# Performance work log

Measured on AMD Instinct MI355X. Metric: run time of the kernel, lower is better.

Reference implementation:

```python
import jax, jax.numpy as jnp
import numpy as np
import math

B, T, C, H = 4, 2048, 1024, 16
D = C // H  # head dim = 64

def setup_inputs() -> dict:
    key = jax.random.key(0)
    k1, k2, k3 = jax.random.split(key, 3)
    scale = 0.02
    return {
        "x": jax.random.normal(k1, (B, T, C), dtype=jnp.float32),
        "W_qkv": jax.random.normal(k2, (C, 3 * C), dtype=jnp.float32) * scale,
        "b_qkv": jnp.zeros((3 * C,), dtype=jnp.float32),
        "W_proj": jax.random.normal(k3, (C, C), dtype=jnp.float32) * scale,
        "b_proj": jnp.zeros((C,), dtype=jnp.float32),
    }

def reference(x, W_qkv, b_qkv, W_proj, b_proj):
    Bx, Tx, Cx = x.shape
    qkv = x @ W_qkv + b_qkv                      # [B, T, 3C]
    q, k, v = jnp.split(qkv, 3, axis=-1)
    # [B, T, C] -> [B, H, T, D]
    q = q.reshape(Bx, Tx, H, D).transpose(0, 2, 1, 3)
    k = k.reshape(Bx, Tx, H, D).transpose(0, 2, 1, 3)
    v = v.reshape(Bx, Tx, H, D).transpose(0, 2, 1, 3)
    scores = jnp.einsum("bhqd,bhkd->bhqk", q, k) * (1.0 / math.sqrt(D))
    causal = jnp.tril(jnp.ones((Tx, Tx), dtype=bool))  # [T, T]
    scores = jnp.where(causal[None, None, :, :], scores, jnp.finfo(scores.dtype).min)
    attn = jax.nn.softmax(scores, axis=-1)
    # dropout(p=0.1) in the original is stochastic; omitted for a deterministic baseline
    out = jnp.einsum("bhqk,bhkd->bhqd", attn, v)   # [B, H, T, D]
    out = out.transpose(0, 2, 1, 3).reshape(Bx, Tx, Cx)
    return out @ W_proj + b_proj
```

## Files before the change

### kernel.cpp

```cpp
#include <hip/hip_runtime.h>
#include <hip/hip_bf16.h>
#include <cstdint>
#include <cstddef>

#define Bsz 4
#define Tseq 2048
#define Cdim 1024
#define Hh 16
#define Dh 64

typedef unsigned short u16;
typedef __bf16 bfx8 __attribute__((ext_vector_type(8)));
typedef float f32x4 __attribute__((ext_vector_type(4)));
typedef float f32x16 __attribute__((ext_vector_type(16)));
typedef unsigned short u16x8 __attribute__((ext_vector_type(8)));

#define AS1 __attribute__((address_space(1)))
#define AS3 __attribute__((address_space(3)))

#define QSCALE 0.18033688f

__device__ __forceinline__ u16 f2b(float f) {
  union { float f; unsigned u; } x; x.f = f;
  unsigned r = x.u + 0x7FFFu + ((x.u >> 16) & 1u);
  return (u16)(r >> 16);
}
__device__ __forceinline__ float b2f(u16 b) {
  union { unsigned u; float f; } x; x.u = ((unsigned)b) << 16; return x.f;
}
__device__ __forceinline__ unsigned cvtpk(float lo, float hi) {
  unsigned r;
  asm("v_cvt_pk_bf16_f32 %0, %1, %2" : "=v"(r) : "v"(lo), "v"(hi));
  return r;
}
__device__ __forceinline__ void swap32(unsigned &a, unsigned &b) {
  asm("v_permlane32_swap_b32 %0, %1" : "+v"(a), "+v"(b));
}

__global__ __launch_bounds__(256) void cvt_f32_bf16(const float* __restrict__ in,
                                                    u16* __restrict__ out, int n4) {
  int i = blockIdx.x * 256 + threadIdx.x;
  if (i < n4) {
    const float4 v = reinterpret_cast<const float4*>(in)[i];
    ushort4 o;
    o.x = f2b(v.x); o.y = f2b(v.y); o.z = f2b(v.z); o.w = f2b(v.w);
    reinterpret_cast<ushort4*>(out)[i] = o;
  }
}

__global__ __launch_bounds__(256) void transpose_cvt(const float* __restrict__ in,
                                                     u16* __restrict__ out, int R, int Cn) {
  __shared__ float tile[32][33];
  const int c0 = blockIdx.x * 32, r0 = blockIdx.y * 32;
  const int tx = threadIdx.x, ty = threadIdx.y;
  for (int i = ty; i < 32; i += 8)
    tile[i][tx] = in[(size_t)(r0 + i) * Cn + c0 + tx];
  __syncthreads();
  for (int i = ty; i < 32; i += 8)
    out[(size_t)(c0 + i) * R + r0 + tx] = f2b(tile[tx][i]);
}

template<int MODE>
__global__ __launch_bounds__(512, 4) void gemm_bt(const u16* __restrict__ A, const u16* __restrict__ Bt,
                                                  const float* __restrict__ bias, void* __restrict__ Cout,
                                                  u16* __restrict__ vtout,
                                                  int M, int N, int K) {
  __shared__ __align__(16) u16 Alds[3][4096];
  __shared__ __align__(16) u16 Blds[3][8192];
  const int tid = threadIdx.x;
  const int lane = tid & 63;
  const int wid = tid >> 6;
  const int nwgx = gridDim.x;
  const int nwg = nwgx * gridDim.y;
  int lin = blockIdx.y * nwgx + blockIdx.x;
  lin = (lin & 7) * (nwg >> 3) + (lin >> 3);
  const int mbase = (lin / nwgx) * 128;
  const int nbase = (lin % nwgx) * 256;
  const int wm = wid & 1, wn = wid >> 1;

  const int sLlow = lane >> 3;
  const int s8 = (lane & 7) ^ sLlow;
  const int srow = 2 * (wid * 8 + sLlow) + (s8 >> 2);
  const int skof = (s8 & 3) * 8;

  const u16* pa  = A  + (size_t)(mbase + srow) * K + skof;
  const u16* pb0 = Bt + (size_t)(nbase + srow) * K + skof;
  const u16* pb1 = pb0 + (size_t)128 * K;

  const int raA = wm * 64 + (lane & 15);
  const int LA = raA >> 1;
  const int pA = ((raA & 1) * 4 + (lane >> 4)) ^ (LA & 7);
  const int aoffw = LA * 64 + pA * 8;
  const int rbB = wn * 64 + (lane & 15);
  const int LB = rbB >> 1;
  const int pB = ((rbB & 1) * 4 + (lane >> 4)) ^ (LB & 7);
  const int boffw = LB * 64 + pB * 8;

  AS3 u16* aldsb = (AS3 u16*)&Alds[0][0];
  AS3 u16* bldsb = (AS3 u16*)&Blds[0][0];

  const f32x4 vzero = {0.f, 0.f, 0.f, 0.f};
  f32x4 acc[4][4];
  #pragma unroll
  for (int i = 0; i < 4; ++i)
    #pragma unroll
    for (int j = 0; j < 4; ++j) acc[i][j] = vzero;

  const int NT = K >> 5;

  auto stage = [&](int slot) {
    __builtin_amdgcn_global_load_lds((AS1 void*)const_cast<u16*>(pa),
                                     (AS3 void*)&Alds[slot][wid * 512], 16, 0, 0);
    __builtin_amdgcn_global_load_lds((AS1 void*)const_cast<u16*>(pb0),
                                     (AS3 void*)&Blds[slot][wid * 512], 16, 0, 0);
    __builtin_amdgcn_global_load_lds((AS1 void*)const_cast<u16*>(pb1),
                                     (AS3 void*)&Blds[slot][4096 + wid * 512], 16, 0, 0);
    pa += 32; pb0 += 32; pb1 += 32;
  };

  stage(0);
  stage(1);
  asm volatile("s_waitcnt vmcnt(3)" ::: "memory");
  __builtin_amdgcn_s_barrier();

  int slot = 0, pf = 2;
  for (int t = 0; t < NT; ++t) {
    if (t + 2 < NT) stage(pf);

    bfx8 af[4], bfv[4];
    {
      AS3 u16* ap = aldsb + slot * 4096 + aoffw;
      AS3 u16* bp = bldsb + slot * 8192 + boffw;
      asm volatile("ds_read_b128 %0, %1"             : "=v"(af[0])  : "v"(ap));
      asm volatile("ds_read_b128 %0, %1 offset:1024" : "=v"(af[1])  : "v"(ap));
      asm volatile("ds_read_b128 %0, %1"             : "=v"(bfv[0]) : "v"(bp));
      asm volatile("ds_read_b128 %0, %1 offset:1024" : "=v"(bfv[1]) : "v"(bp));
      asm volatile("ds_read_b128 %0, %1 offset:2048" : "=v"(bfv[2]) : "v"(bp));
      asm volatile("ds_read_b128 %0, %1 offset:3072" : "=v"(bfv[3]) : "v"(bp));
      asm volatile("ds_read_b128 %0, %1 offset:2048" : "=v"(af[2])  : "v"(ap));
      asm volatile("ds_read_b128 %0, %1 offset:3072" : "=v"(af[3])  : "v"(ap));
    }
    asm volatile("s_waitcnt lgkmcnt(2)" ::: "memory");
    __builtin_amdgcn_sched_barrier(0);

    __builtin_amdgcn_s_setprio(1);
    #pragma unroll
    for (int mf = 0; mf < 2; ++mf)
      #pragma unroll
      for (int nf = 0; nf < 4; ++nf)
        acc[mf][nf] = __builtin_amdgcn_mfma_f32_16x16x32_bf16(af[mf], bfv[nf], acc[mf][nf], 0, 0, 0);
    __builtin_amdgcn_s_setprio(0);

    asm volatile("s_waitcnt lgkmcnt(0)" ::: "memory");
    __builtin_amdgcn_sched_barrier(0);

    __builtin_amdgcn_s_setprio(1);
    #pragma unroll
    for (int mf = 2; mf < 4; ++mf)
      #pragma unroll
      for (int nf = 0; nf < 4; ++nf)
        acc[mf][nf] = __builtin_amdgcn_mfma_f32_16x16x32_bf16(af[mf], bfv[nf], acc[mf][nf], 0, 0, 0);
    __builtin_amdgcn_s_setprio(0);

    if (t + 2 < NT)      { asm volatile("s_waitcnt vmcnt(3)" ::: "memory"); }
    else if (t + 1 < NT) { asm volatile("s_waitcnt vmcnt(0)" ::: "memory"); }
    if (t + 1 < NT) __builtin_amdgcn_s_barrier();

    slot = (slot == 2) ? 0 : slot + 1;
    pf   = (pf == 2) ? 0 : pf + 1;
  }

  float bv[4];
  #pragma unroll
  for (int nf = 0; nf < 4; ++nf) bv[nf] = bias[nbase + wn * 64 + nf * 16 + (lane & 15)];
  #pragma unroll
  for (int mf = 0; mf < 4; ++mf) {
    #pragma unroll
    for (int nf = 0; nf < 4; ++nf) {
      const int r0 = mbase + wm * 64 + mf * 16 + (lane >> 4) * 4;
      const int c  = nbase + wn * 64 + nf * 16 + (lane & 15);
      const int cb = nbase + wn * 64 + nf * 16;
      const float cscale = (MODE == 1 && cb >= 1024 && cb < 2048) ? QSCALE : 1.0f;
      float v[4];
      #pragma unroll
      for (int j = 0; j < 4; ++j) v[j] = (acc[mf][nf][j] + bv[nf]) * cscale;
      if (MODE == 1 && cb >= 2048) {
        const int hh = (c - 2048) >> 6, dd = (c - 2048) & 63;
        const int bb = r0 >> 11, tt = r0 & 2047;
        ushort4 pkd;
        pkd.x = f2b(v[0]); pkd.y = f2b(v[1]); pkd.z = f2b(v[2]); pkd.w = f2b(v[3]);
        *reinterpret_cast<ushort4*>(
            &vtout[(((size_t)bb * Hh + hh) * Dh + dd) * Tseq + tt]) = pkd;
      } else {
        #pragma unroll
        for (int j = 0; j < 4; ++j) {
          if (MODE == 1) ((u16*)Cout)[(size_t)(r0 + j) * N + c] = f2b(v[j]);
          else           ((float*)Cout)[(size_t)(r0 + j) * N + c] = v[j];
        }
      }
    }
  }
}

#define ROWI(r) (((r) & 3) + 8 * ((r) >> 2))
__global__ __launch_bounds__(512, 4) void attn_fwd(const u16* __restrict__ qkv,
                                                   const u16* __restrict__ vt,
                                                   u16* __restrict__ aout) {
  __shared__ __align__(16) u16 Klds[4][64 * 64];
  __shared__ __align__(16) u16 Vtlds[4][64 * 64];
  const int tid = threadIdx.x;
  const int lane = tid & 63;
  const int wid = tid >> 6;
  const int qg = wid & 3;
  const int half = wid >> 2;
  const int lin = blockIdx.y * gridDim.x + blockIdx.x;
  const int bh = (lin & 7) * 8 + ((lin >> 3) & 7);
  const int qpair = lin >> 6;
  const int b = bh >> 4, h = bh & 15;
  const int hi4 = (lane & 32) >> 3;

  const int stg_row = lane >> 3;
  const int stg_srcslot = (lane & 7) ^ (stg_row & 7);

  const u16* gkbase = qkv + ((size_t)b * Tseq + wid * 8 + stg_row) * 3072
                      + 1024 + h * 64 + stg_srcslot * 8;
  const u16* gvbase = vt + ((size_t)bh * Dh + wid * 8 + stg_row) * Tseq + stg_srcslot * 8;

  float* Olds = reinterpret_cast<float*>(&Klds[0][0]);
  float* Llds = reinterpret_cast<float*>(&Vtlds[0][0]);

  #pragma unroll 1
  for (int pass = 0; pass < 2; ++pass) {
    const int qtile = pass ? qpair : (15 - qpair);
    const int qwb = qtile * 128 + qg * 32;
    const int ntiles = qtile * 2 + 2;

    bfx8 qf[4];
    {
      const int qrow = qwb + (lane & 31);
      #pragma unroll
      for (int c = 0; c < 4; ++c) {
        const u16* src = qkv + (size_t)(b * Tseq + qrow) * 3072 + h * 64 + c * 16 + (hi4 << 1);
        qf[c] = *reinterpret_cast<const bfx8*>(src);
      }
    }

    float l_r = 0.f;
    f32x16 o0, o1;
    #pragma unroll
    for (int r = 0; r < 16; ++r) { o0[r] = 0.f; o1[r] = 0.f; }

    auto stageT = [&](int t) {
      const u16* gk = gkbase + (size_t)t * 64 * 3072;
      const u16* gv = gvbase + t * 64;
      __builtin_amdgcn_global_load_lds((AS1 void*)const_cast<u16*>(gk),
                                       (AS3 void*)&Klds[t & 3][wid * 512], 16, 0, 0);
      __builtin_amdgcn_global_load_lds((AS1 void*)const_cast<u16*>(gv),
                                       (AS3 void*)&Vtlds[t & 3][wid * 512], 16, 0, 0);
    };
    stageT(0);
    stageT(1);
    __syncthreads();

    for (int t = 0; t < ntiles; t += 2) {
      if (t + 2 < ntiles) stageT(t + 2);
      if (t + 3 < ntiles) stageT(t + 3);

      const int tt = t + half;
      const int kb = tt * 64;
      const int buf = tt & 3;
      if (kb <= qwb + 31) {
        f32x16 st0, st1;
        #pragma unroll
        for (int r = 0; r < 16; ++r) { st0[r] = 0.f; st1[r] = 0.f; }
        __builtin_amdgcn_s_setprio(1);
        #pragma unroll
        for (int c = 0; c < 4; ++c) {
          const int row0 = lane & 31;
          const int sl = (c * 2 + (lane >> 5)) ^ (row0 & 7);
          const bfx8 k0 = *reinterpret_cast<const bfx8*>(&Klds[buf][row0 * 64 + sl * 8]);
          const bfx8 k1 = *reinterpret_cast<const bfx8*>(&Klds[buf][(row0 + 32) * 64 + sl * 8]);
          st0 = __builtin_amdgcn_mfma_f32_32x32x16_bf16(k0, qf[c], st0, 0, 0, 0);
          st1 = __builtin_amdgcn_mfma_f32_32x32x16_bf16(k1, qf[c], st1, 0, 0, 0);
        }
        __builtin_amdgcn_s_setprio(0);

        if (kb + 63 > qwb) {
          const int qg_ = qwb + (lane & 31);
          #pragma unroll
          for (int r = 0; r < 16; ++r) {
            const int kt = kb + ROWI(r) + hi4;
            if (kt > qg_) st0[r] = -1e30f;
            if (kt + 32 > qg_) st1[r] = -1e30f;
          }
        }

        float rs = 0.f;
        #pragma unroll
        for (int r = 0; r < 16; ++r) { st0[r] = exp2f(st0[r]); rs += st0[r]; }
        #pragma unroll
        for (int r = 0; r < 16; ++r) { st1[r] = exp2f(st1[r]); rs += st1[r]; }
        rs += __shfl_xor(rs, 32);
        l_r += rs;

        bfx8 pf[4];
        #pragma unroll
        for (int tph = 0; tph < 2; ++tph) {
          #pragma unroll
          for (int c2 = 0; c2 < 2; ++c2) {
            const int rb = c2 * 8;
            float s0 = tph ? st1[rb + 0] : st0[rb + 0], s1 = tph ? st1[rb + 1] : st0[rb + 1];
            float s2 = tph ? st1[rb + 2] : st0[rb + 2], s3 = tph ? st1[rb + 3] : st0[rb + 3];
            float s4 = tph ? st1[rb + 4] : st0[rb + 4], s5 = tph ? st1[rb + 5] : st0[rb + 5];
            float s6 = tph ? st1[rb + 6] : st0[rb + 6], s7 = tph ? st1[rb + 7] : st0[rb + 7];
            unsigned w0 = cvtpk(s0, s1);
            unsigned w2 = cvtpk(s4, s5);
            swap32(w0, w2);
            unsigned w1 = cvtpk(s2, s3);
            unsigned w3 = cvtpk(s6, s7);
            swap32(w1, w3);
            union { unsigned w[4]; bfx8 v; } u;
            u.w[0] = w0; u.w[1] = w1; u.w[2] = w2; u.w[3] = w3;
            pf[tph * 2 + c2] = u.v;
          }
        }

        __builtin_amdgcn_s_setprio(1);
        #pragma unroll
        for (int c4 = 0; c4 < 4; ++c4) {
          const int vrow = lane & 31;
          const int sl = (c4 * 2 + (lane >> 5)) ^ (vrow & 7);
          const bfx8 vf0 = *reinterpret_cast<const bfx8*>(&Vtlds[buf][vrow * 64 + sl * 8]);
          const bfx8 vf1 = *reinterpret_cast<const bfx8*>(&Vtlds[buf][(vrow + 32) * 64 + sl * 8]);
          o0 = __builtin_amdgcn_mfma_f32_32x32x16_bf16(pf[c4], vf0, o0, 0, 0, 0);
          o1 = __builtin_amdgcn_mfma_f32_32x32x16_bf16(pf[c4], vf1, o1, 0, 0, 0);
        }
        __builtin_amdgcn_s_setprio(0);
      }

      __syncthreads();
    }

    if (half == 1) {
      Llds[qg * 64 + lane] = l_r;
      #pragma unroll
      for (int r = 0; r < 16; ++r) {
        Olds[qg * 2048 + r * 64 + lane]        = o0[r];
        Olds[qg * 2048 + (r + 16) * 64 + lane] = o1[r];
      }
    }
    __syncthreads();
    if (half == 0) {
      const float l1 = Llds[qg * 64 + lane];
      const float linv = 1.0f / (l_r + l1);
      #pragma unroll
      for (int r = 0; r < 16; ++r) {
        const int src = ROWI(r) + hi4;
        const float cr = __shfl(linv, src);
        const int q = qwb + src;
        const float v0 = (o0[r] + Olds[qg * 2048 + r * 64 + lane]) * cr;
        const float v1 = (o1[r] + Olds[qg * 2048 + (r + 16) * 64 + lane]) * cr;
        aout[(size_t)(b * Tseq + q) * 1024 + h * 64 + (lane & 31)]      = f2b(v0);
        aout[(size_t)(b * Tseq + q) * 1024 + h * 64 + 32 + (lane & 31)] = f2b(v1);
      }
    }
    __syncthreads();
  }
}

extern "C" void kernel_launch(void* const* d_in, const int* in_sizes, int n_in,
                              void* d_out, int out_size, void* d_ws, size_t ws_size,
                              hipStream_t stream) {
  const float* x      = (const float*)d_in[0];
  const float* W_qkv  = (const float*)d_in[1];
  const float* b_qkv  = (const float*)d_in[2];
  const float* W_proj = (const float*)d_in[3];
  const float* b_proj = (const float*)d_in[4];
  float* out = (float*)d_out;

  char* ws = (char*)d_ws;
  const size_t SZ_XB    = 16777216;
  const size_t SZ_WQKV  = 6291456;
  const size_t SZ_WPROJ = 2097152;
  const size_t SZ_QKV   = 50331648;
  u16* xb     = (u16*)ws;
  u16* wqkvT  = (u16*)(ws + SZ_XB);
  u16* wprojT = (u16*)(ws + SZ_XB + SZ_WQKV);
  u16* qkv    = (u16*)(ws + SZ_XB + SZ_WQKV + SZ_WPROJ);
  u16* vt     = (u16*)(ws + SZ_XB + SZ_WQKV + SZ_WPROJ + SZ_QKV);

  cvt_f32_bf16<<<dim3((Bsz * Tseq * Cdim / 4 + 255) / 256), dim3(256), 0, stream>>>(
      x, xb, Bsz * Tseq * Cdim / 4);
  transpose_cvt<<<dim3(3 * Cdim / 32, Cdim / 32), dim3(32, 8), 0, stream>>>(W_qkv, wqkvT, Cdim, 3 * Cdim);
  transpose_cvt<<<dim3(Cdim / 32, Cdim / 32), dim3(32, 8), 0, stream>>>(W_proj, wprojT, Cdim, Cdim);
  gemm_bt<1><<<dim3(3 * Cdim / 256, Bsz * Tseq / 128), dim3(512), 0, stream>>>(
      xb, wqkvT, b_qkv, qkv, vt, Bsz * Tseq, 3 * Cdim, Cdim);
  attn_fwd<<<dim3(8, Bsz * Hh), dim3(512), 0, stream>>>(qkv, vt, xb);
  gemm_bt<0><<<dim3(Cdim / 256, Bsz * Tseq / 128), dim3(512), 0, stream>>>(
      xb, wprojT, b_proj, out, nullptr, Bsz * Tseq, Cdim, Cdim);
}
```

Measured before the change: 166.6 us.

## Use 4-wave GEMM workgroups with 128x64 per-wave tiles

The bf16 GEMM now runs 256-thread workgroups (4 waves) instead of 512, and each wave computes a full 128x64 output slab with 8x4 MFMA accumulators. Each thread issues six global-to-LDS loads per stage instead of three, and the wait counts change to match. The aim is more register-level reuse of A fragments and less LDS read traffic per MFMA. The cost is doubled accumulator registers, occupancy limited to 2 workgroups, and fewer waves available to hide latency.

New measurement: 168.7 us. Within noise of the previous version (+1.2%).

```diff
diff --git a/kernel.cpp b/kernel.cpp
--- a/kernel.cpp
+++ b/kernel.cpp
@@ -61,7 +61,7 @@
 }
 
 template<int MODE>
-__global__ __launch_bounds__(512, 4) void gemm_bt(const u16* __restrict__ A, const u16* __restrict__ Bt,
+__global__ __launch_bounds__(256, 2) void gemm_bt(const u16* __restrict__ A, const u16* __restrict__ Bt,
                                                   const float* __restrict__ bias, void* __restrict__ Cout,
                                                   u16* __restrict__ vtout,
                                                   int M, int N, int K) {
@@ -76,58 +76,66 @@
   lin = (lin & 7) * (nwg >> 3) + (lin >> 3);
   const int mbase = (lin / nwgx) * 128;
   const int nbase = (lin % nwgx) * 256;
-  const int wm = wid & 1, wn = wid >> 1;
-
-  const int sLlow = lane >> 3;
-  const int s8 = (lane & 7) ^ sLlow;
-  const int srow = 2 * (wid * 8 + sLlow) + (s8 >> 2);
+
+  const int sL = tid >> 3;
+  const int s8 = (tid & 7) ^ (sL & 7);
+  const int srow = 2 * sL + (s8 >> 2);
   const int skof = (s8 & 3) * 8;
 
-  const u16* pa  = A  + (size_t)(mbase + srow) * K + skof;
+  const u16* pa0 = A  + (size_t)(mbase + srow) * K + skof;
+  const u16* pa1 = pa0 + (size_t)64 * K;
   const u16* pb0 = Bt + (size_t)(nbase + srow) * K + skof;
-  const u16* pb1 = pb0 + (size_t)128 * K;
-
-  const int raA = wm * 64 + (lane & 15);
-  const int LA = raA >> 1;
-  const int pA = ((raA & 1) * 4 + (lane >> 4)) ^ (LA & 7);
+  const u16* pb1 = pb0 + (size_t)64 * K;
+  const u16* pb2 = pb0 + (size_t)128 * K;
+  const u16* pb3 = pb0 + (size_t)192 * K;
+
+  const int ra0 = lane & 15;
+  const int LA = ra0 >> 1;
+  const int pA = ((ra0 & 1) * 4 + (lane >> 4)) ^ (LA & 7);
   const int aoffw = LA * 64 + pA * 8;
-  const int rbB = wn * 64 + (lane & 15);
-  const int LB = rbB >> 1;
-  const int pB = ((rbB & 1) * 4 + (lane >> 4)) ^ (LB & 7);
+  const int rb0 = wid * 64 + (lane & 15);
+  const int LB = rb0 >> 1;
+  const int pB = ((rb0 & 1) * 4 + (lane >> 4)) ^ (LB & 7);
   const int boffw = LB * 64 + pB * 8;
 
   AS3 u16* aldsb = (AS3 u16*)&Alds[0][0];
   AS3 u16* bldsb = (AS3 u16*)&Blds[0][0];
 
   const f32x4 vzero = {0.f, 0.f, 0.f, 0.f};
-  f32x4 acc[4][4];
+  f32x4 acc[8][4];
   #pragma unroll
-  for (int i = 0; i < 4; ++i)
+  for (int i = 0; i < 8; ++i)
     #pragma unroll
     for (int j = 0; j < 4; ++j) acc[i][j] = vzero;
 
   const int NT = K >> 5;
 
   auto stage = [&](int slot) {
-    __builtin_amdgcn_global_load_lds((AS1 void*)const_cast<u16*>(pa),
-                                     (AS3 void*)&Alds[slot][wid * 512], 16, 0, 0);
+    __builtin_amdgcn_global_load_lds((AS1 void*)const_cast<u16*>(pa0),
+                                     (AS3 void*)&Alds[slot][tid * 8], 16, 0, 0);
+    __builtin_amdgcn_global_load_lds((AS1 void*)const_cast<u16*>(pa1),
+                                     (AS3 void*)&Alds[slot][2048 + tid * 8], 16, 0, 0);
     __builtin_amdgcn_global_load_lds((AS1 void*)const_cast<u16*>(pb0),
-                                     (AS3 void*)&Blds[slot][wid * 512], 16, 0, 0);
+                                     (AS3 void*)&Blds[slot][tid * 8], 16, 0, 0);
     __builtin_amdgcn_global_load_lds((AS1 void*)const_cast<u16*>(pb1),
-                                     (AS3 void*)&Blds[slot][4096 + wid * 512], 16, 0, 0);
-    pa += 32; pb0 += 32; pb1 += 32;
+                                     (AS3 void*)&Blds[slot][2048 + tid * 8], 16, 0, 0);
+    __builtin_amdgcn_global_load_lds((AS1 void*)const_cast<u16*>(pb2),
+                                     (AS3 void*)&Blds[slot][4096 + tid * 8], 16, 0, 0);
+    __builtin_amdgcn_global_load_lds((AS1 void*)const_cast<u16*>(pb3),
+                                     (AS3 void*)&Blds[slot][6144 + tid * 8], 16, 0, 0);
+    pa0 += 32; pa1 += 32; pb0 += 32; pb1 += 32; pb2 += 32; pb3 += 32;
   };
 
   stage(0);
   stage(1);
-  asm volatile("s_waitcnt vmcnt(3)" ::: "memory");
+  asm volatile("s_waitcnt vmcnt(6)" ::: "memory");
   __builtin_amdgcn_s_barrier();
 
   int slot = 0, pf = 2;
   for (int t = 0; t < NT; ++t) {
     if (t + 2 < NT) stage(pf);
 
-    bfx8 af[4], bfv[4];
+    bfx8 af[8], bfv[4];
     {
       AS3 u16* ap = aldsb + slot * 4096 + aoffw;
       AS3 u16* bp = bldsb + slot * 8192 + boffw;
@@ -139,8 +147,12 @@
       asm volatile("ds_read_b128 %0, %1 offset:3072" : "=v"(bfv[3]) : "v"(bp));
       asm volatile("ds_read_b128 %0, %1 offset:2048" : "=v"(af[2])  : "v"(ap));
       asm volatile("ds_read_b128 %0, %1 offset:3072" : "=v"(af[3])  : "v"(ap));
-    }
-    asm volatile("s_waitcnt lgkmcnt(2)" ::: "memory");
+      asm volatile("ds_read_b128 %0, %1 offset:4096" : "=v"(af[4])  : "v"(ap));
+      asm volatile("ds_read_b128 %0, %1 offset:5120" : "=v"(af[5])  : "v"(ap));
+      asm volatile("ds_read_b128 %0, %1 offset:6144" : "=v"(af[6])  : "v"(ap));
+      asm volatile("ds_read_b128 %0, %1 offset:7168" : "=v"(af[7])  : "v"(ap));
+    }
+    asm volatile("s_waitcnt lgkmcnt(6)" ::: "memory");
     __builtin_amdgcn_sched_barrier(0);
 
     __builtin_amdgcn_s_setprio(1);
@@ -156,13 +168,13 @@
 
     __builtin_amdgcn_s_setprio(1);
     #pragma unroll
-    for (int mf = 2; mf < 4; ++mf)
+    for (int mf = 2; mf < 8; ++mf)
       #pragma unroll
       for (int nf = 0; nf < 4; ++nf)
         acc[mf][nf] = __builtin_amdgcn_mfma_f32_16x16x32_bf16(af[mf], bfv[nf], acc[mf][nf], 0, 0, 0);
     __builtin_amdgcn_s_setprio(0);
 
-    if (t + 2 < NT)      { asm volatile("s_waitcnt vmcnt(3)" ::: "memory"); }
+    if (t + 2 < NT)      { asm volatile("s_waitcnt vmcnt(6)" ::: "memory"); }
     else if (t + 1 < NT) { asm volatile("s_waitcnt vmcnt(0)" ::: "memory"); }
     if (t + 1 < NT) __builtin_amdgcn_s_barrier();
 
@@ -172,14 +184,14 @@
 
   float bv[4];
   #pragma unroll
-  for (int nf = 0; nf < 4; ++nf) bv[nf] = bias[nbase + wn * 64 + nf * 16 + (lane & 15)];
+  for (int nf = 0; nf < 4; ++nf) bv[nf] = bias[nbase + wid * 64 + nf * 16 + (lane & 15)];
   #pragma unroll
-  for (int mf = 0; mf < 4; ++mf) {
+  for (int mf = 0; mf < 8; ++mf) {
     #pragma unroll
     for (int nf = 0; nf < 4; ++nf) {
-      const int r0 = mbase + wm * 64 + mf * 16 + (lane >> 4) * 4;
-      const int c  = nbase + wn * 64 + nf * 16 + (lane & 15);
-      const int cb = nbase + wn * 64 + nf * 16;
+      const int r0 = mbase + mf * 16 + (lane >> 4) * 4;
+      const int c  = nbase + wid * 64 + nf * 16 + (lane & 15);
+      const int cb = nbase + wid * 64 + nf * 16;
       const float cscale = (MODE == 1 && cb >= 1024 && cb < 2048) ? QSCALE : 1.0f;
       float v[4];
       #pragma unroll
@@ -393,9 +405,9 @@
       x, xb, Bsz * Tseq * Cdim / 4);
   transpose_cvt<<<dim3(3 * Cdim / 32, Cdim / 32), dim3(32, 8), 0, stream>>>(W_qkv, wqkvT, Cdim, 3 * Cdim);
   transpose_cvt<<<dim3(Cdim / 32, Cdim / 32), dim3(32, 8), 0, stream>>>(W_proj, wprojT, Cdim, Cdim);
-  gemm_bt<1><<<dim3(3 * Cdim / 256, Bsz * Tseq / 128), dim3(512), 0, stream>>>(
+  gemm_bt<1><<<dim3(3 * Cdim / 256, Bsz * Tseq / 128), dim3(256), 0, stream>>>(
       xb, wqkvT, b_qkv, qkv, vt, Bsz * Tseq, 3 * Cdim, Cdim);
   attn_fwd<<<dim3(8, Bsz * Hh), dim3(512), 0, stream>>>(qkv, vt, xb);
-  gemm_bt<0><<<dim3(Cdim / 256, Bsz * Tseq / 128), dim3(512), 0, stream>>>(
+  gemm_bt<0><<<dim3(Cdim / 256, Bsz * Tseq / 128), dim3(256), 0, stream>>>(
       xb, wprojT, b_proj, out, nullptr, Bsz * Tseq, Cdim, Cdim);
 }
```

## Add dedicated 256x256-tile QKV GEMM with 4-slot LDS pipeline

Applied to the files above, without the earlier changes.

Replaces the generic 128x256 gemm_bt for the QKV projection with a specialized kernel using 256x256 output tiles, a four-slot LDS ring filled by direct global-to-LDS loads, and half-tile MFMA phases. Each wave now computes a 128x64 sub-tile, which raises arithmetic intensity and halves redundant B-tile loads. In exchange, occupancy drops to launch_bounds(512,2) with heavier register and LDS use. The grid is only 12x32 workgroups, which may leave some compute units underused. Bias, Q scaling and the V-transpose epilogue are kept.

New measurement: 178.3 us. 1.07x slower.

```diff
diff --git a/kernel.cpp b/kernel.cpp
--- a/kernel.cpp
+++ b/kernel.cpp
@@ -58,6 +58,177 @@
   __syncthreads();
   for (int i = ty; i < 32; i += 8)
     out[(size_t)(c0 + i) * R + r0 + tx] = f2b(tile[tx][i]);
+}
+
+__global__ __launch_bounds__(512, 2) void gemm_qkv(const u16* __restrict__ A, const u16* __restrict__ Bt,
+                                                   const float* __restrict__ bias, u16* __restrict__ Cout,
+                                                   u16* __restrict__ vtout,
+                                                   int M, int N, int K) {
+  __shared__ __align__(16) u16 Alds[4][8192];
+  __shared__ __align__(16) u16 Blds[4][8192];
+  const int tid = threadIdx.x;
+  const int lane = tid & 63;
+  const int wid = tid >> 6;
+  const int nwgx = gridDim.x;
+  const int nwg = nwgx * gridDim.y;
+  int lin = blockIdx.y * nwgx + blockIdx.x;
+  lin = (lin & 7) * (nwg >> 3) + (lin >> 3);
+  const int mbase = (lin / nwgx) * 256;
+  const int nbase = (lin % nwgx) * 256;
+  const int wm = wid & 1, wn = wid >> 1;
+
+  const int s8 = (lane & 7) ^ ((lane >> 3) & 7);
+  const int growb = wid * 16 + 2 * (lane >> 3) + (s8 >> 2);
+  const int skof = (s8 & 3) * 8;
+  const u16* paw = A  + (size_t)(mbase + growb) * K + skof;
+  const u16* pbw = Bt + (size_t)(nbase + growb) * K + skof;
+  const size_t rstep128 = (size_t)128 * K;
+
+  const int rowA = wm * 128 + (lane & 15);
+  const int LA = rowA >> 1;
+  const int aoff = LA * 64 + ((((rowA & 1) << 2) + (lane >> 4)) ^ (LA & 7)) * 8;
+  const int rowB = wn * 64 + (lane & 15);
+  const int LB = rowB >> 1;
+  const int boff = LB * 64 + ((((rowB & 1) << 2) + (lane >> 4)) ^ (LB & 7)) * 8;
+
+  AS3 u16* aldsb = (AS3 u16*)&Alds[0][0];
+  AS3 u16* bldsb = (AS3 u16*)&Blds[0][0];
+
+  const f32x4 vzero = {0.f, 0.f, 0.f, 0.f};
+  f32x4 acc[8][4];
+  #pragma unroll
+  for (int i = 0; i < 8; ++i)
+    #pragma unroll
+    for (int j = 0; j < 4; ++j) acc[i][j] = vzero;
+
+  const int NT = K >> 6;
+  const int KH = NT * 2;
+
+  auto stA = [&](int kh, int slot) {
+    const u16* p = paw + kh * 32;
+    __builtin_amdgcn_global_load_lds((AS1 void*)const_cast<u16*>(p),
+                                     (AS3 void*)&Alds[slot][wid * 512], 16, 0, 0);
+    __builtin_amdgcn_global_load_lds((AS1 void*)const_cast<u16*>(p + rstep128),
+                                     (AS3 void*)&Alds[slot][4096 + wid * 512], 16, 0, 0);
+  };
+  auto stB = [&](int kh, int slot) {
+    const u16* p = pbw + kh * 32;
+    __builtin_amdgcn_global_load_lds((AS1 void*)const_cast<u16*>(p),
+                                     (AS3 void*)&Blds[slot][wid * 512], 16, 0, 0);
+    __builtin_amdgcn_global_load_lds((AS1 void*)const_cast<u16*>(p + rstep128),
+                                     (AS3 void*)&Blds[slot][4096 + wid * 512], 16, 0, 0);
+  };
+
+  bfx8 af[4], bfv[4];
+  auto rdA0 = [&](int slot) {
+    AS3 u16* ap = aldsb + slot * 8192 + aoff;
+    asm volatile("ds_read_b128 %0, %1"             : "=v"(af[0]) : "v"(ap));
+    asm volatile("ds_read_b128 %0, %1 offset:1024" : "=v"(af[1]) : "v"(ap));
+    asm volatile("ds_read_b128 %0, %1 offset:2048" : "=v"(af[2]) : "v"(ap));
+    asm volatile("ds_read_b128 %0, %1 offset:3072" : "=v"(af[3]) : "v"(ap));
+  };
+  auto rdA1 = [&](int slot) {
+    AS3 u16* ap = aldsb + slot * 8192 + aoff;
+    asm volatile("ds_read_b128 %0, %1 offset:4096" : "=v"(af[0]) : "v"(ap));
+    asm volatile("ds_read_b128 %0, %1 offset:5120" : "=v"(af[1]) : "v"(ap));
+    asm volatile("ds_read_b128 %0, %1 offset:6144" : "=v"(af[2]) : "v"(ap));
+    asm volatile("ds_read_b128 %0, %1 offset:7168" : "=v"(af[3]) : "v"(ap));
+  };
+  auto rdB = [&](int slot) {
+    AS3 u16* bp = bldsb + slot * 8192 + boff;
+    asm volatile("ds_read_b128 %0, %1"             : "=v"(bfv[0]) : "v"(bp));
+    asm volatile("ds_read_b128 %0, %1 offset:1024" : "=v"(bfv[1]) : "v"(bp));
+    asm volatile("ds_read_b128 %0, %1 offset:2048" : "=v"(bfv[2]) : "v"(bp));
+    asm volatile("ds_read_b128 %0, %1 offset:3072" : "=v"(bfv[3]) : "v"(bp));
+  };
+
+  #define QKV_MFMA(MH)                                                                          \
+    __builtin_amdgcn_s_setprio(1);                                                              \
+    _Pragma("unroll")                                                                           \
+    for (int i = 0; i < 4; ++i)                                                                 \
+      _Pragma("unroll")                                                                         \
+      for (int nf = 0; nf < 4; ++nf)                                                            \
+        acc[(MH) * 4 + i][nf] =                                                                 \
+            __builtin_amdgcn_mfma_f32_16x16x32_bf16(af[i], bfv[nf], acc[(MH) * 4 + i][nf],      \
+                                                    0, 0, 0);                                   \
+    __builtin_amdgcn_s_setprio(0);
+
+  stA(0, 0); stB(0, 0);
+  stA(1, 1); stB(1, 1);
+  stA(2, 2); stB(2, 2);
+  asm volatile("s_waitcnt vmcnt(4)" ::: "memory");
+  __builtin_amdgcn_s_barrier();
+
+  for (int t = 0; t < NT; ++t) {
+    const int g = 2 * t;
+    const int sk0 = g & 3, sk1 = (g + 1) & 3;
+    const int sp0 = (g + 3) & 3, sp1 = (g + 4) & 3;
+
+    rdA0(sk0); rdB(sk0);
+    if (g + 3 < KH) { stA(g + 3, sp0); stB(g + 3, sp0); }
+    __builtin_amdgcn_s_barrier();
+    asm volatile("s_waitcnt lgkmcnt(0)" ::: "memory");
+    __builtin_amdgcn_sched_barrier(0);
+    QKV_MFMA(0);
+    __builtin_amdgcn_s_barrier();
+
+    rdA1(sk0);
+    __builtin_amdgcn_s_barrier();
+    asm volatile("s_waitcnt lgkmcnt(0)" ::: "memory");
+    __builtin_amdgcn_sched_barrier(0);
+    QKV_MFMA(1);
+    __builtin_amdgcn_s_barrier();
+
+    rdA0(sk1); rdB(sk1);
+    if (g + 4 < KH) { stA(g + 4, sp1); stB(g + 4, sp1); }
+    __builtin_amdgcn_s_barrier();
+    asm volatile("s_waitcnt lgkmcnt(0)" ::: "memory");
+    __builtin_amdgcn_sched_barrier(0);
+    QKV_MFMA(0);
+    __builtin_amdgcn_s_barrier();
+
+    rdA1(sk1);
+    __builtin_amdgcn_s_barrier();
+    asm volatile("s_waitcnt lgkmcnt(0)" ::: "memory");
+    __builtin_amdgcn_sched_barrier(0);
+    QKV_MFMA(1);
+
+    if (t + 1 < NT) {
+      if (t + 2 < NT) { asm volatile("s_waitcnt vmcnt(4)" ::: "memory"); }
+      else            { asm volatile("s_waitcnt vmcnt(0)" ::: "memory"); }
+      __builtin_amdgcn_s_barrier();
+    }
+  }
+  #undef QKV_MFMA
+
+  float bv[4];
+  #pragma unroll
+  for (int nf = 0; nf < 4; ++nf) bv[nf] = bias[nbase + wn * 64 + nf * 16 + (lane & 15)];
+  #pragma unroll
+  for (int mf = 0; mf < 8; ++mf) {
+    #pragma unroll
+    for (int nf = 0; nf < 4; ++nf) {
+      const int r0 = mbase + wm * 128 + mf * 16 + (lane >> 4) * 4;
+      const int c  = nbase + wn * 64 + nf * 16 + (lane & 15);
+      const int cb = nbase + wn * 64 + nf * 16;
+      const float cscale = (cb >= 1024 && cb < 2048) ? QSCALE : 1.0f;
+      float v[4];
+      #pragma unroll
+      for (int j = 0; j < 4; ++j) v[j] = (acc[mf][nf][j] + bv[nf]) * cscale;
+      if (cb >= 2048) {
+        const int hh = (c - 2048) >> 6, dd = (c - 2048) & 63;
+        const int bb = r0 >> 11, tt = r0 & 2047;
+        ushort4 pkd;
+        pkd.x = f2b(v[0]); pkd.y = f2b(v[1]); pkd.z = f2b(v[2]); pkd.w = f2b(v[3]);
+        *reinterpret_cast<ushort4*>(
+            &vtout[(((size_t)bb * Hh + hh) * Dh + dd) * Tseq + tt]) = pkd;
+      } else {
+        #pragma unroll
+        for (int j = 0; j < 4; ++j)
+          Cout[(size_t)(r0 + j) * N + c] = f2b(v[j]);
+      }
+    }
+  }
 }
 
 template<int MODE>
@@ -393,7 +564,7 @@
       x, xb, Bsz * Tseq * Cdim / 4);
   transpose_cvt<<<dim3(3 * Cdim / 32, Cdim / 32), dim3(32, 8), 0, stream>>>(W_qkv, wqkvT, Cdim, 3 * Cdim);
   transpose_cvt<<<dim3(Cdim / 32, Cdim / 32), dim3(32, 8), 0, stream>>>(W_proj, wprojT, Cdim, Cdim);
-  gemm_bt<1><<<dim3(3 * Cdim / 256, Bsz * Tseq / 128), dim3(512), 0, stream>>>(
+  gemm_qkv<<<dim3(3 * Cdim / 256, Bsz * Tseq / 256), dim3(512), 0, stream>>>(
       xb, wqkvT, b_qkv, qkv, vt, Bsz * Tseq, 3 * Cdim, Cdim);
   attn_fwd<<<dim3(8, Bsz * Hh), dim3(512), 0, stream>>>(qkv, vt, xb);
   gemm_bt<0><<<dim3(Cdim / 256, Bsz * Tseq / 128), dim3(512), 0, stream>>>(
```
